# Kernel optimization log

Measured on AMD Instinct MI355X. Metric: run time of the kernel, lower is better.

The kernel has to match this reference:

```python
import jax, jax.numpy as jnp
import numpy as np

B, N, CACHE = 2, 2048, 512
D_MODEL, N_HEADS, HEAD_DIM, FF, KSZ = 768, 12, 64, 3072, 31
EPS = 1e-5


def rmsnorm(x, w):
    return x * jax.lax.rsqrt(jnp.mean(x * x, axis=-1, keepdims=True) + EPS) * w


def rope(x, pos):
    # x: [B, T, H, D], pos: [T] (absolute positions incl. cache offset)
    half = x.shape[-1] // 2
    inv = 1.0 / (10000.0 ** (jnp.arange(half, dtype=jnp.float32) / half))
    ang = pos.astype(jnp.float32)[:, None] * inv[None, :]           # [T, half]
    cos = jnp.concatenate([jnp.cos(ang), jnp.cos(ang)], -1)[None, :, None, :]
    sin = jnp.concatenate([jnp.sin(ang), jnp.sin(ang)], -1)[None, :, None, :]
    x1, x2 = x[..., :half], x[..., half:]
    rot = jnp.concatenate([-x2, x1], -1)
    return x * cos + rot * sin


def setup_inputs() -> dict:
    key = jax.random.key(0)
    ks = jax.random.split(key, 16)
    w = lambda k, shape: jax.random.normal(k, shape, jnp.float32) * 0.02
    kk = jax.random.split(ks[15], 16)
    return {
        "x": jax.random.normal(ks[0], (B, N, D_MODEL), jnp.float32),
        "attn_mask": jnp.ones((B, CACHE + N), bool),
        "pad_mask": jnp.zeros((B, N), bool),
        "length": N,
        "cached_kv": jax.random.normal(ks[1], (B, CACHE, 2, N_HEADS, HEAD_DIM), jnp.float32),
        "ff1_norm_w": jnp.ones((D_MODEL,), jnp.float32),
        "ff1_w1": w(ks[2], (D_MODEL, FF)), "ff1_b1": jnp.zeros((FF,), jnp.float32),
        "ff1_w2": w(ks[3], (FF, D_MODEL)), "ff1_b2": jnp.zeros((D_MODEL,), jnp.float32),
        "attn_norm_w": jnp.ones((D_MODEL,), jnp.float32),
        "qkv_w": w(ks[4], (D_MODEL, 3 * N_HEADS * HEAD_DIM)),
        "out_w": w(ks[5], (N_HEADS * HEAD_DIM, D_MODEL)),
        "q_norm_w": jnp.ones((HEAD_DIM,), jnp.float32),
        "k_norm_w": jnp.ones((HEAD_DIM,), jnp.float32),
        "conv_norm_w": jnp.ones((D_MODEL,), jnp.float32),
        "pw1_w": w(ks[6], (D_MODEL, 2 * D_MODEL)), "pw1_b": jnp.zeros((2 * D_MODEL,), jnp.float32),
        "dw_w": w(ks[7], (D_MODEL, KSZ)), "dw_b": jnp.zeros((D_MODEL,), jnp.float32),
        "bn_g": jnp.ones((D_MODEL,), jnp.float32), "bn_b": jnp.zeros((D_MODEL,), jnp.float32),
        "pw2_w": w(ks[8], (D_MODEL, D_MODEL)), "pw2_b": jnp.zeros((D_MODEL,), jnp.float32),
        "ff2_norm_w": jnp.ones((D_MODEL,), jnp.float32),
        "ff2_w1": w(kk[0], (D_MODEL, FF)), "ff2_b1": jnp.zeros((FF,), jnp.float32),
        "ff2_w2": w(kk[1], (FF, D_MODEL)), "ff2_b2": jnp.zeros((D_MODEL,), jnp.float32),
        "out_norm_w": jnp.ones((D_MODEL,), jnp.float32),
    }


def _ff(x, nw, w1, b1, w2, b2):
    h = jax.nn.gelu(rmsnorm(x, nw) @ w1 + b1)        # FusedMLP: gelu(tanh approx)
    return 0.5 * (h @ w2 + b2)                        # Scale(0.5, ...)


def _attention(x, pad_mask, attn_mask, cached_kv, nw, qkv_w, out_w, qnw, knw):
    y = rmsnorm(x, nw)
    y = jnp.where(pad_mask[..., None], 0.0, y)
    qkv = (y @ qkv_w).reshape(B, N, N_HEADS, HEAD_DIM, 3)  # (h d qkv) layout
    q, k, v = qkv[..., 0], qkv[..., 1], qkv[..., 2]
    q = rmsnorm(q, qnw)
    k = rmsnorm(k, knw)
    k_full = jnp.concatenate([cached_kv[:, :, 0], k], axis=1)  # [B, KV, H, D]
    v_full = jnp.concatenate([cached_kv[:, :, 1], v], axis=1)
    kv_to_cache = jnp.stack([k_full, v_full], axis=2)          # [B, KV, 2, H, D]
    kv_len = k_full.shape[1]
    pos = jnp.arange(kv_len)
    k_rot = rope(k_full, pos)
    q_rot = rope(q, pos[kv_len - N:])
    scale = 1.0 / jnp.sqrt(jnp.asarray(HEAD_DIM, jnp.float32))
    scores = jnp.einsum('bqhd,bkhd->bhqk', q_rot, k_rot) * scale
    scores = jnp.where(attn_mask[:, None, None, :], scores, jnp.finfo(scores.dtype).min)
    attn = jax.nn.softmax(scores, axis=-1)
    out = jnp.einsum('bhqk,bkhd->bqhd', attn, v_full).reshape(B, N, N_HEADS * HEAD_DIM)
    out = jnp.where(pad_mask[..., None], 0.0, out)
    return out @ out_w, kv_to_cache


def _conv(x, pad_mask, nw, pw1_w, pw1_b, dw_w, dw_b, bn_g, bn_b, pw2_w, pw2_b):
    y = rmsnorm(x, nw)
    y = jnp.where(pad_mask[..., None], 0.0, y)
    y = y @ pw1_w + pw1_b                             # pointwise conv1
    a, b = jnp.split(y, 2, axis=-1)
    y = a * jax.nn.sigmoid(b)                          # GLU
    rhs = dw_w.T[:, None, :]                           # [K, 1, C] (WIO, depthwise)
    y = jax.lax.conv_general_dilated(
        y, rhs, (1,), [(KSZ // 2, KSZ // 2)],
        dimension_numbers=('NWC', 'WIO', 'NWC'),
        feature_group_count=D_MODEL) + dw_b
    m = jnp.mean(y, axis=(0, 1))                       # batch(re)norm, train-mode stats
    v = jnp.var(y, axis=(0, 1))
    y = (y - m) * jax.lax.rsqrt(v + EPS) * bn_g + bn_b
    y = y * jax.nn.sigmoid(y)                          # SiLU
    return y @ pw2_w + pw2_b


def reference(x, attn_mask, pad_mask, length, cached_kv,
              ff1_norm_w, ff1_w1, ff1_b1, ff1_w2, ff1_b2,
              attn_norm_w, qkv_w, out_w, q_norm_w, k_norm_w,
              conv_norm_w, pw1_w, pw1_b, dw_w, dw_b, bn_g, bn_b, pw2_w, pw2_b,
              ff2_norm_w, ff2_w1, ff2_b1, ff2_w2, ff2_b2, out_norm_w):
    x = _ff(x, ff1_norm_w, ff1_w1, ff1_b1, ff1_w2, ff1_b2) + x
    attn_out, kv_to_cache = _attention(x, pad_mask, attn_mask, cached_kv,
                                       attn_norm_w, qkv_w, out_w, q_norm_w, k_norm_w)
    x = attn_out + x
    # NOTE: source code has no residual add around the conv block
    x = _conv(x, pad_mask, conv_norm_w, pw1_w, pw1_b, dw_w, dw_b, bn_g, bn_b, pw2_w, pw2_b)
    x = _ff(x, ff2_norm_w, ff2_w1, ff2_b1, ff2_w2, ff2_b2) + x
    x = rmsnorm(x, out_norm_w)
    return x, kv_to_cache
```

## Files before the change

### kernel.cpp

```cpp
#include <hip/hip_runtime.h>
#include <hip/hip_bf16.h>
#include <math.h>

namespace {
constexpr int Bc   = 2;
constexpr int Nn   = 2048;
constexpr int CACHE= 512;
constexpr int KVL  = 2560;
constexpr int DM   = 768;
constexpr int NH   = 12;
constexpr int HD   = 64;
constexpr int FFD  = 3072;
constexpr int RR   = Bc * Nn;
}
#define EPSF 1e-5f

typedef unsigned short u16;
typedef __bf16 bf16x8 __attribute__((ext_vector_type(8)));
typedef float  f32x4  __attribute__((ext_vector_type(4)));
typedef u16    u16x8  __attribute__((ext_vector_type(8)));
typedef u16    u16x4  __attribute__((ext_vector_type(4)));

#define GPTR(p) ((const __attribute__((address_space(1))) void*)(p))
#define LPTR(p) ((__attribute__((address_space(3))) void*)(p))

__device__ __forceinline__ float fast_exp2(float a) {
  float e;
  asm("v_exp_f32 %0, %1" : "=v"(e) : "v"(a));
  return e;
}
__device__ __forceinline__ float fast_rcp(float x) {
  float r;
  asm("v_rcp_f32 %0, %1" : "=v"(r) : "v"(x));
  return r;
}
__device__ __forceinline__ float geluf(float x) {
  const float u = 0.7978845608028654f * x * (1.0f + 0.044715f * x * x);
  const float e = fast_exp2(u * 2.885390081777927f);
  const float t = (e - 1.0f) * fast_rcp(e + 1.0f);
  return 0.5f * x * (1.0f + t);
}
__device__ __forceinline__ float sigmoidf_(float x) {
  const float e = fast_exp2(-x * 1.4426950408889634f);
  return fast_rcp(1.0f + e);
}
__device__ __forceinline__ u16 f2bf(float x) {
  union { float f; unsigned u; } v; v.f = x;
  unsigned r = (v.u + 0x7fffu + ((v.u >> 16) & 1u)) >> 16;
  return (u16)r;
}
__device__ __forceinline__ float bf2f(u16 u) {
  union { unsigned u; float f; } v; v.u = ((unsigned)u) << 16;
  return v.f;
}
__device__ __forceinline__ void rope_sc(float pos, int j, float* s, float* c) {
  const float e = fast_exp2(-(float)j * 0.41524101186092028f);
  const float rev = pos * (e * 0.15915494309189535f);
  const float fr = rev - floorf(rev);
  asm("v_sin_f32 %0, %1" : "=v"(*s) : "v"(fr));
  asm("v_cos_f32 %0, %1" : "=v"(*c) : "v"(fr));
}

template<bool BF>
__global__ __launch_bounds__(256) void k_rmsnorm2(const float* __restrict__ in,
                                                  const float* __restrict__ w,
                                                  void* __restrict__ outv) {
  const int row = blockIdx.x;
  const int t = threadIdx.x;
  const float4* x4 = (const float4*)(in + (size_t)row * DM);
  float4 v = make_float4(0.f, 0.f, 0.f, 0.f);
  float ss = 0.f;
  if (t < 192) {
    v = x4[t];
    ss = fmaf(v.x, v.x, fmaf(v.y, v.y, fmaf(v.z, v.z, v.w * v.w)));
  }
  __shared__ float red[5];
#pragma unroll
  for (int off = 32; off > 0; off >>= 1) ss += __shfl_down(ss, off, 64);
  if ((t & 63) == 0) red[t >> 6] = ss;
  __syncthreads();
  if (t == 0) red[4] = red[0] + red[1] + red[2] + red[3];
  __syncthreads();
  const float scale = rsqrtf(red[4] * (1.0f / (float)DM) + EPSF);
  if (t < 192) {
    const float4 wv = ((const float4*)w)[t];
    const float r0 = v.x * scale * wv.x;
    const float r1 = v.y * scale * wv.y;
    const float r2 = v.z * scale * wv.z;
    const float r3 = v.w * scale * wv.w;
    if (BF) {
      u16x4 o; o[0] = f2bf(r0); o[1] = f2bf(r1); o[2] = f2bf(r2); o[3] = f2bf(r3);
      ((u16x4*)outv)[(size_t)row * 192 + t] = o;
    } else {
      ((float4*)outv)[(size_t)row * 192 + t] = make_float4(r0, r1, r2, r3);
    }
  }
}

__device__ __forceinline__ void wt_tile(const float* __restrict__ W,
                                        u16* __restrict__ Wt, int K, int N,
                                        int gx, int r,
                                        u16 (*T)[72], int tid) {
  const int nb = (r % gx) * 64;
  const int kb = (r / gx) * 64;
#pragma unroll
  for (int p = 0; p < 4; ++p) {
    const int rr = p * 16 + (tid >> 4);
    const int c = (tid & 15) * 4;
    float4 v = *(const float4*)(W + (size_t)(kb + rr) * N + nb + c);
    T[c + 0][rr] = f2bf(v.x); T[c + 1][rr] = f2bf(v.y);
    T[c + 2][rr] = f2bf(v.z); T[c + 3][rr] = f2bf(v.w);
  }
  __syncthreads();
  const int cc = (tid & 7) * 8;
#pragma unroll
  for (int p = 0; p < 2; ++p) {
    const int rr = p * 32 + (tid >> 3);
    *(u16x8*)(Wt + (size_t)(nb + rr) * K + kb + cc) = *(const u16x8*)&T[rr][cc];
  }
}

__global__ __launch_bounds__(256) void k_wt_all(
    const float* w0, u16* o0,
    const float* w1, u16* o1,
    const float* w2, u16* o2,
    const float* w3, u16* o3,
    const float* w4, u16* o4,
    const float* w5, u16* o5,
    const float* w6, u16* o6,
    const float* w7, u16* o7,
    float* stats) {
  __shared__ __align__(16) u16 T[64][72];
  const int tid = threadIdx.x;
  int r = blockIdx.x;
  if (r < 576) { wt_tile(w0, o0, 768, 3072, 48, r, T, tid); return; } r -= 576;
  if (r < 576) { wt_tile(w1, o1, 3072, 768, 12, r, T, tid); return; } r -= 576;
  if (r < 432) { wt_tile(w2, o2, 768, 2304, 36, r, T, tid); return; } r -= 432;
  if (r < 144) { wt_tile(w3, o3, 768, 768, 12, r, T, tid); return; } r -= 144;
  if (r < 288) { wt_tile(w4, o4, 768, 1536, 24, r, T, tid); return; } r -= 288;
  if (r < 144) { wt_tile(w5, o5, 768, 768, 12, r, T, tid); return; } r -= 144;
  if (r < 576) { wt_tile(w6, o6, 768, 3072, 48, r, T, tid); return; } r -= 576;
  if (r < 576) { wt_tile(w7, o7, 3072, 768, 12, r, T, tid); return; } r -= 576;
  const int idx = r * 256 + tid;
  if (idx < 2 * DM) stats[idx] = 0.f;
}

template<int BM, int BN, int BKt, int MODE, bool OUTBF>
__global__ __launch_bounds__(256) void k_gemm_mfma(const u16* __restrict__ A,
                                                   const u16* __restrict__ Wt,
                                                   const float* __restrict__ bias,
                                                   const float* __restrict__ res,
                                                   void* __restrict__ Cv,
                                                   int K, int Nc) {
  constexpr int CH  = BKt / 8;
  constexpr int SWM = CH - 1;
  constexpr int RT  = BM / 32;
  constexpr int CT  = BN / 32;
  constexpr int KK  = BKt / 32;
  constexpr int ACH = BM * BKt / 8 / 256;
  constexpr int BCH = BN * BKt / 8 / 256;
  constexpr int LD  = ACH + BCH;
  static_assert(LD == 3 || LD == 4, "vmcnt ledger");
  __shared__ __align__(16) u16 As[3][BM * BKt];
  __shared__ __align__(16) u16 Bs[3][BN * BKt];
  const int tid  = threadIdx.x;
  const int lane = tid & 63;
  const int wbase = tid & 192;
  const int w    = tid >> 6;
  const int gx = gridDim.x;
  const int nwg = gx * gridDim.y;
  int bid = blockIdx.y * gx + blockIdx.x;
  if ((nwg & 7) == 0) bid = (bid & 7) * (nwg >> 3) + (bid >> 3);
  const int rowBase = (bid / gx) * BM;
  const int colBase = (bid % gx) * BN;
  const int l15 = lane & 15, quad = lane >> 4;
  const int wr = w >> 1, wc = w & 1;
  const int xsw = l15 & SWM;

  const u16* aS[ACH];
#pragma unroll
  for (int s = 0; s < ACH; ++s) {
    const int c = s * 256 + tid;
    const int r = c / CH;
    const int kc = (c & SWM) ^ (r & SWM);
    aS[s] = A + (size_t)(rowBase + r) * K + kc * 8;
  }
  const u16* bS[BCH];
#pragma unroll
  for (int s = 0; s < BCH; ++s) {
    const int c = s * 256 + tid;
    const int r = c / CH;
    const int kc = (c & SWM) ^ (r & SWM);
    bS[s] = Wt + (size_t)(colBase + r) * K + kc * 8;
  }

  f32x4 acc[RT][CT];
#pragma unroll
  for (int i = 0; i < RT; ++i)
#pragma unroll
    for (int j = 0; j < CT; ++j) acc[i][j] = (f32x4){0.f, 0.f, 0.f, 0.f};

  auto stage = [&](int buf, int k0e) {
#pragma unroll
    for (int s = 0; s < ACH; ++s)
      __builtin_amdgcn_global_load_lds(GPTR(aS[s] + k0e),
          LPTR((char*)As[buf] + (size_t)(s * 256 + wbase) * 16), 16, 0, 0);
#pragma unroll
    for (int s = 0; s < BCH; ++s)
      __builtin_amdgcn_global_load_lds(GPTR(bS[s] + k0e),
          LPTR((char*)Bs[buf] + (size_t)(s * 256 + wbase) * 16), 16, 0, 0);
  };

#define GEMM_STEP(BUF, I, DOSTAGE, LAST)                                           \
  {                                                                                \
    if (LAST) { asm volatile("s_waitcnt vmcnt(0)" ::: "memory"); }                 \
    else if (LD == 3) { asm volatile("s_waitcnt vmcnt(3)" ::: "memory"); }         \
    else { asm volatile("s_waitcnt vmcnt(4)" ::: "memory"); }                      \
    __builtin_amdgcn_s_barrier();                                                  \
    asm volatile("" ::: "memory");                                                 \
    if (DOSTAGE) stage(((BUF) + 2) % 3, ((I) + 2) * BKt);                          \
    const u16* ab = As[BUF];                                                       \
    const u16* bb = Bs[BUF];                                                       \
    _Pragma("unroll")                                                              \
    for (int kk = 0; kk < KK; ++kk) {                                              \
      bf16x8 aF[RT], bF[CT];                                                       \
      _Pragma("unroll")                                                            \
      for (int rt = 0; rt < RT; ++rt) {                                            \
        const int m = wr * (BM / 2) + rt * 16 + l15;                               \
        aF[rt] = *(const bf16x8*)&ab[m * BKt + (((kk * 4 + quad) ^ xsw) * 8)];     \
      }                                                                            \
      _Pragma("unroll")                                                            \
      for (int ct = 0; ct < CT; ++ct) {                                            \
        const int n = wc * (BN / 2) + ct * 16 + l15;                               \
        bF[ct] = *(const bf16x8*)&bb[n * BKt + (((kk * 4 + quad) ^ xsw) * 8)];     \
      }                                                                            \
      _Pragma("unroll")                                                            \
      for (int rt = 0; rt < RT; ++rt)                                              \
        _Pragma("unroll")                                                          \
        for (int ct = 0; ct < CT; ++ct)                                            \
          acc[rt][ct] = __builtin_amdgcn_mfma_f32_16x16x32_bf16(bF[ct], aF[rt],    \
                                                                acc[rt][ct],       \
                                                                0, 0, 0);          \
    }                                                                              \
  }

  const int nsteps = K / BKt;
  stage(0, 0);
  stage(1, BKt);
  int i = 0;
  for (; i < nsteps - 3; i += 3) {
    GEMM_STEP(0, i + 0, true, false);
    GEMM_STEP(1, i + 1, true, false);
    GEMM_STEP(2, i + 2, true, false);
  }
  GEMM_STEP(0, nsteps - 3, true, false);
  GEMM_STEP(1, nsteps - 2, false, false);
  GEMM_STEP(2, nsteps - 1, false, true);
#undef GEMM_STEP

#pragma unroll
  for (int ct = 0; ct < CT; ++ct) {
    const int n0 = colBase + wc * (BN / 2) + ct * 16 + quad * 4;
    float b0 = 0.f, b1 = 0.f, b2 = 0.f, b3 = 0.f;
    if (bias) {
      const float4 bv = *(const float4*)(bias + n0);
      b0 = bv.x; b1 = bv.y; b2 = bv.z; b3 = bv.w;
    }
#pragma unroll
    for (int rt = 0; rt < RT; ++rt) {
      const int m = rowBase + wr * (BM / 2) + rt * 16 + l15;
      float v0 = acc[rt][ct][0] + b0;
      float v1 = acc[rt][ct][1] + b1;
      float v2 = acc[rt][ct][2] + b2;
      float v3 = acc[rt][ct][3] + b3;
      if (MODE == 1) {
        v0 = geluf(v0); v1 = geluf(v1); v2 = geluf(v2); v3 = geluf(v3);
      } else if (MODE == 2) {
        const float4 rv = *(const float4*)(res + (size_t)m * Nc + n0);
        v0 = 0.5f * v0 + rv.x; v1 = 0.5f * v1 + rv.y;
        v2 = 0.5f * v2 + rv.z; v3 = 0.5f * v3 + rv.w;
      } else if (MODE == 3) {
        const float4 rv = *(const float4*)(res + (size_t)m * Nc + n0);
        v0 += rv.x; v1 += rv.y; v2 += rv.z; v3 += rv.w;
      }
      if (OUTBF) {
        unsigned w0, w1;
        asm("v_cvt_pk_bf16_f32 %0, %1, %2" : "=v"(w0) : "v"(v0), "v"(v1));
        asm("v_cvt_pk_bf16_f32 %0, %1, %2" : "=v"(w1) : "v"(v2), "v"(v3));
        uint2 st; st.x = w0; st.y = w1;
        *(uint2*)((u16*)Cv + (size_t)m * Nc + n0) = st;
      } else {
        *(float4*)((float*)Cv + (size_t)m * Nc + n0) =
            make_float4(v0, v1, v2, v3);
      }
    }
  }
}

__global__ __launch_bounds__(768) void k_qkv_post(const float* __restrict__ qkv,
                                                  const float* __restrict__ qw,
                                                  const float* __restrict__ kw,
                                                  u16* __restrict__ qbf,
                                                  u16* __restrict__ krotbf,
                                                  float* __restrict__ kvout) {
  const int row = blockIdx.x;
  const int b = row >> 11;
  const int n = row & 2047;
  const int h = threadIdx.x >> 6;
  const int d = threadIdx.x & 63;
  const float* src = qkv + (size_t)row * (3 * DM) + h * 192 + d * 3;
  const float q = src[0], k = src[1], v = src[2];
  float sq = q * q, sk = k * k;
#pragma unroll
  for (int off = 32; off > 0; off >>= 1) {
    sq += __shfl_xor(sq, off, 64);
    sk += __shfl_xor(sk, off, 64);
  }
  const float qs = rsqrtf(sq * (1.0f / 64.0f) + EPSF);
  const float ks = rsqrtf(sk * (1.0f / 64.0f) + EPSF);
  const float qn = q * qs * qw[d];
  const float kn = k * ks * kw[d];
  const size_t kvbase = ((size_t)b * KVL + (CACHE + n)) * (2 * DM) + h * 64 + d;
  kvout[kvbase] = kn;
  kvout[kvbase + DM] = v;
  const int j = d & 31;
  float s, c;
  rope_sc((float)(CACHE + n), j, &s, &c);
  const float oq = __shfl_xor(qn, 32, 64);
  const float ok = __shfl_xor(kn, 32, 64);
  const float rq = (d < 32) ? -oq : oq;
  const float rk = (d < 32) ? -ok : ok;
  qbf[((size_t)row * NH + h) * 64 + d] = f2bf((qn * c + rq * s) * 0.18033688011112042f);
  krotbf[((size_t)(b * KVL + CACHE + n) * NH + h) * 64 + d] = f2bf(kn * c + rk * s);
}

__global__ __launch_bounds__(768) void k_cache_prep(const float* __restrict__ cached,
                                                    float* __restrict__ kvout,
                                                    u16* __restrict__ krotbf) {
  const int row = blockIdx.x;
  const int b = row / CACHE, t = row - b * CACHE;
  const int h = threadIdx.x >> 6;
  const int d = threadIdx.x & 63;
  const float k = cached[((size_t)row * 2 + 0) * DM + h * 64 + d];
  const float v = cached[((size_t)row * 2 + 1) * DM + h * 64 + d];
  const size_t kb = ((size_t)b * KVL + t) * (2 * DM) + h * 64 + d;
  kvout[kb] = k;
  kvout[kb + DM] = v;
  const int j = d & 31;
  float s, c;
  rope_sc((float)t, j, &s, &c);
  const float ok = __shfl_xor(k, 32, 64);
  const float rk = (d < 32) ? -ok : ok;
  krotbf[((size_t)(b * KVL + t) * NH + h) * 64 + d] = f2bf(k * c + rk * s);
}

__global__ __launch_bounds__(256) void k_vt(const float* __restrict__ kvout,
                                            u16* __restrict__ vtbf) {
  __shared__ __align__(16) u16 T[64][72];
  const int bh = blockIdx.x / 40;
  const int tb = blockIdx.x % 40;
  const int b = bh / NH, h = bh % NH;
  const int t0 = tb * 64;
  {
    const int tloc = threadIdx.x >> 2;
    const int dg = (threadIdx.x & 3) * 16;
    const float* src = kvout + ((size_t)b * KVL + t0 + tloc) * (2 * DM) + DM + h * 64 + dg;
    float4 v0 = *(const float4*)(src);
    float4 v1 = *(const float4*)(src + 4);
    float4 v2 = *(const float4*)(src + 8);
    float4 v3 = *(const float4*)(src + 12);
    T[dg + 0][tloc] = f2bf(v0.x);  T[dg + 1][tloc] = f2bf(v0.y);
    T[dg + 2][tloc] = f2bf(v0.z);  T[dg + 3][tloc] = f2bf(v0.w);
    T[dg + 4][tloc] = f2bf(v1.x);  T[dg + 5][tloc] = f2bf(v1.y);
    T[dg + 6][tloc] = f2bf(v1.z);  T[dg + 7][tloc] = f2bf(v1.w);
    T[dg + 8][tloc] = f2bf(v2.x);  T[dg + 9][tloc] = f2bf(v2.y);
    T[dg + 10][tloc] = f2bf(v2.z); T[dg + 11][tloc] = f2bf(v2.w);
    T[dg + 12][tloc] = f2bf(v3.x); T[dg + 13][tloc] = f2bf(v3.y);
    T[dg + 14][tloc] = f2bf(v3.z); T[dg + 15][tloc] = f2bf(v3.w);
  }
  __syncthreads();
  const int d = threadIdx.x >> 2;
  const int kg = (threadIdx.x & 3) * 16;
  u16x8 a = *(const u16x8*)&T[d][kg];
  u16x8 b8 = *(const u16x8*)&T[d][kg + 8];
  u16* dst = vtbf + ((size_t)(b * NH + h) * 64 + d) * KVL + t0 + kg;
  *(u16x8*)dst = a;
  *(u16x8*)(dst + 8) = b8;
}

__global__ __launch_bounds__(256) void k_attn3(const u16* __restrict__ qbf,
                                               const u16* __restrict__ krotbf,
                                               const u16* __restrict__ vtbf,
                                               u16* __restrict__ attnout) {
  __shared__ __align__(16) char smem[49152];
  u16* const KsB = (u16*)smem;
  u16* const VsB = (u16*)(smem + 24576);
  const int lane = threadIdx.x & 63;
  const int wid  = threadIdx.x >> 6;
  const int bid = blockIdx.x;
  const int swz = (bid & 7) * (768 / 8) + (bid >> 3);
  const int qblk = swz & 31;
  const int bh   = swz >> 5;
  const int b = bh / NH, h = bh % NH;
  const int q0 = qblk * 64 + wid * 16;
  const int l15 = lane & 15;
  const int quad = lane >> 4;
  const int sw = l15 & 7;

  const u16* qp = qbf + ((size_t)(b * Nn + q0 + l15) * NH + h) * 64 + quad * 8;
  const bf16x8 bQ0 = *(const bf16x8*)qp;
  const bf16x8 bQ1 = *(const bf16x8*)(qp + 32);
  asm volatile("" :: "v"(*(const f32x4*)&bQ0), "v"(*(const f32x4*)&bQ1));

  f32x4 O[4] = {};
  float l_lane = 0.f;

  const int c0 = (wid * 2 + 0) * 64 + lane;
  const int c1 = (wid * 2 + 1) * 64 + lane;
  const int r0 = c0 >> 3, kc0 = (c0 & 7) ^ (r0 & 7);
  const int r1 = c1 >> 3, kc1 = (c1 & 7) ^ (r1 & 7);
  const int g0 = (r0 & 3) | ((r0 & 0xC) << 1) | ((r0 & 0x10) >> 2) | (r0 & 0x20);
  const int g1 = (r1 & 3) | ((r1 & 0xC) << 1) | ((r1 & 0x10) >> 2) | (r1 & 0x20);
  const u16* kbase = krotbf + ((size_t)b * KVL * NH + h) * 64;
  const u16* vbase = vtbf + ((size_t)(b * NH + h) * 64) * KVL;
  const u16* ksrc0 = kbase + (size_t)g0 * (NH * 64) + kc0 * 8;
  const u16* ksrc1 = kbase + (size_t)g1 * (NH * 64) + kc1 * 8;
  const u16* vsrc0 = vbase + (size_t)r0 * KVL + kc0 * 8;
  const u16* vsrc1 = vbase + (size_t)r1 * KVL + kc1 * 8;
  const size_t kd0 = (size_t)(wid * 2 + 0) * 1024;
  const size_t kd1 = (size_t)(wid * 2 + 1) * 1024;

  auto stage = [&](int buf, int tile) {
    char* kd = (char*)KsB + buf * 8192;
    char* vd = (char*)VsB + buf * 8192;
    const size_t koff = (size_t)tile * (64 * NH * 64);
    const int voff = tile * 64;
    __builtin_amdgcn_global_load_lds(GPTR(ksrc0 + koff), LPTR(kd + kd0), 16, 0, 0);
    __builtin_amdgcn_global_load_lds(GPTR(vsrc0 + voff), LPTR(vd + kd0), 16, 0, 0);
    __builtin_amdgcn_global_load_lds(GPTR(ksrc1 + koff), LPTR(kd + kd1), 16, 0, 0);
    __builtin_amdgcn_global_load_lds(GPTR(vsrc1 + voff), LPTR(vd + kd1), 16, 0, 0);
  };

#define ATTN_TILE(BI, I, DOSTAGE, LAST)                                            \
  {                                                                                \
    if (LAST) { asm volatile("s_waitcnt vmcnt(0)" ::: "memory"); }                 \
    else      { asm volatile("s_waitcnt vmcnt(4)" ::: "memory"); }                 \
    __builtin_amdgcn_s_barrier();                                                  \
    asm volatile("" ::: "memory");                                                 \
    if (DOSTAGE) stage(((BI) + 2) % 3, (I) + 2);                                   \
    const u16* ksc = KsB + (BI) * 4096;                                            \
    const u16* vsc = VsB + (BI) * 4096;                                            \
    unsigned Pr[2][4];                                                             \
    _Pragma("unroll")                                                              \
    for (int nt = 0; nt < 4; ++nt) {                                               \
      const int krow = nt * 16 + l15;                                              \
      const bf16x8 aK0 = *(const bf16x8*)&ksc[krow * 64 + ((quad ^ sw) * 8)];      \
      const bf16x8 aK1 = *(const bf16x8*)&ksc[krow * 64 + (((4 + quad) ^ sw) * 8)];\
      f32x4 cc = {};                                                               \
      cc = __builtin_amdgcn_mfma_f32_16x16x32_bf16(aK0, bQ0, cc, 0, 0, 0);         \
      cc = __builtin_amdgcn_mfma_f32_16x16x32_bf16(aK1, bQ1, cc, 0, 0, 0);         \
      const float p0 = fast_exp2(cc[0]);                                           \
      const float p1 = fast_exp2(cc[1]);                                           \
      const float p2 = fast_exp2(cc[2]);                                           \
      const float p3 = fast_exp2(cc[3]);                                           \
      l_lane += (p0 + p1) + (p2 + p3);                                             \
      asm("v_cvt_pk_bf16_f32 %0, %1, %2"                                           \
          : "=v"(Pr[nt >> 1][(nt & 1) * 2 + 0]) : "v"(p0), "v"(p1));               \
      asm("v_cvt_pk_bf16_f32 %0, %1, %2"                                           \
          : "=v"(Pr[nt >> 1][(nt & 1) * 2 + 1]) : "v"(p2), "v"(p3));               \
    }                                                                              \
    __builtin_amdgcn_s_setprio(1);                                                 \
    _Pragma("unroll")                                                              \
    for (int kt = 0; kt < 2; ++kt) {                                               \
      union { unsigned u[4]; bf16x8 v; } pu;                                       \
      pu.u[0] = Pr[kt][0]; pu.u[1] = Pr[kt][1];                                    \
      pu.u[2] = Pr[kt][2]; pu.u[3] = Pr[kt][3];                                    \
      _Pragma("unroll")                                                            \
      for (int ot = 0; ot < 4; ++ot) {                                             \
        const int vrow = ot * 16 + l15;                                            \
        const bf16x8 aV =                                                          \
            *(const bf16x8*)&vsc[vrow * 64 + (((kt * 4 + quad) ^ sw) * 8)];        \
        O[ot] = __builtin_amdgcn_mfma_f32_16x16x32_bf16(aV, pu.v, O[ot], 0, 0, 0); \
      }                                                                            \
    }                                                                              \
    __builtin_amdgcn_s_setprio(0);                                                 \
  }

  stage(0, 0);
  stage(1, 1);
  for (int j = 0; j < 12; ++j) {
    const int i0 = j * 3;
    ATTN_TILE(0, i0 + 0, true, false);
    ATTN_TILE(1, i0 + 1, true, false);
    ATTN_TILE(2, i0 + 2, true, false);
  }
  ATTN_TILE(0, 36, true, false);
  ATTN_TILE(1, 37, true, false);
  ATTN_TILE(2, 38, false, false);
  ATTN_TILE(0, 39, false, true);
#undef ATTN_TILE

  l_lane += __shfl_xor(l_lane, 16, 64);
  l_lane += __shfl_xor(l_lane, 32, 64);
  const float il = 1.0f / l_lane;
  __builtin_amdgcn_s_barrier();
  asm volatile("" ::: "memory");
  float* const OF  = (float*)smem;
  float* const ILs = (float*)(smem + 17408);
  if (quad == 0) ILs[wid * 16 + l15] = il;
  float* of = OF + (size_t)(wid * 16 + l15) * 68;
#pragma unroll
  for (int ot = 0; ot < 4; ++ot)
    *(f32x4*)&of[ot * 16 + quad * 4] = O[ot];
  asm volatile("s_waitcnt lgkmcnt(0)" ::: "memory");
  const int q  = lane >> 2;
  const int dg = (lane & 3) * 16;
  const float sc = ILs[wid * 16 + q];
  const float* srcp = OF + (size_t)(wid * 16 + q) * 68 + dg;
  unsigned wv[8];
#pragma unroll
  for (int i2 = 0; i2 < 8; ++i2) {
    const float a0 = srcp[2 * i2] * sc;
    const float a1 = srcp[2 * i2 + 1] * sc;
    asm("v_cvt_pk_bf16_f32 %0, %1, %2" : "=v"(wv[i2]) : "v"(a0), "v"(a1));
  }
  u16* dst = attnout + ((size_t)(b * Nn + q0 + q)) * DM + h * 64 + dg;
  uint4 s0; s0.x = wv[0]; s0.y = wv[1]; s0.z = wv[2]; s0.w = wv[3];
  uint4 s1; s1.x = wv[4]; s1.y = wv[5]; s1.z = wv[6]; s1.w = wv[7];
  *(uint4*)dst = s0;
  *(uint4*)(dst + 8) = s1;
}

__global__ __launch_bounds__(256) void k_dwconv2(const u16* __restrict__ pw1,
                                                 const float* __restrict__ w,
                                                 const float* __restrict__ bsd,
                                                 float* __restrict__ out,
                                                 float* __restrict__ stats) {
  __shared__ float S[94][68];
  __shared__ float Wl[31][64];
  const int cb = blockIdx.x * 64;
  const int n0 = blockIdx.y * 64;
  const int b  = blockIdx.z;
  for (int idx = threadIdx.x; idx < 94 * 16; idx += 256) {
    const int r = idx >> 4, cg = (idx & 15) * 4;
    const int n = n0 - 15 + r;
    float4 v = make_float4(0.f, 0.f, 0.f, 0.f);
    if (n >= 0 && n < Nn) {
      const u16* p = pw1 + ((size_t)(b * Nn + n)) * (2 * DM) + cb + cg;
      u16x4 av = *(const u16x4*)(p);
      u16x4 gv = *(const u16x4*)(p + DM);
      v.x = bf2f(av[0]) * sigmoidf_(bf2f(gv[0]));
      v.y = bf2f(av[1]) * sigmoidf_(bf2f(gv[1]));
      v.z = bf2f(av[2]) * sigmoidf_(bf2f(gv[2]));
      v.w = bf2f(av[3]) * sigmoidf_(bf2f(gv[3]));
    }
    *(float4*)&S[r][cg] = v;
  }
  for (int idx = threadIdx.x; idx < 31 * 64; idx += 256) {
    const int c = idx & 63, tap = idx >> 6;
    Wl[tap][c] = w[(size_t)(cb + c) * 31 + tap];
  }
  __syncthreads();

  const int cg  = (threadIdx.x & 15) * 4;
  const int nl0 = threadIdx.x >> 4;
  const float4 b4 = *(const float4*)(bsd + cb + cg);
  float sum[4] = {0.f, 0.f, 0.f, 0.f};
  float sq[4]  = {0.f, 0.f, 0.f, 0.f};
#pragma unroll
  for (int p = 0; p < 4; ++p) {
    const int nl = p * 16 + nl0;
    float a0 = b4.x, a1 = b4.y, a2 = b4.z, a3 = b4.w;
#pragma unroll
    for (int t = 0; t < 31; ++t) {
      const float4 sv = *(const float4*)&S[nl + t][cg];
      const float4 wv = *(const float4*)&Wl[t][cg & 63];
      a0 = fmaf(sv.x, wv.x, a0); a1 = fmaf(sv.y, wv.y, a1);
      a2 = fmaf(sv.z, wv.z, a2); a3 = fmaf(sv.w, wv.w, a3);
    }
    *(float4*)(out + ((size_t)(b * Nn + n0 + nl)) * DM + cb + cg) =
        make_float4(a0, a1, a2, a3);
    sum[0] += a0; sum[1] += a1; sum[2] += a2; sum[3] += a3;
    sq[0] = fmaf(a0, a0, sq[0]); sq[1] = fmaf(a1, a1, sq[1]);
    sq[2] = fmaf(a2, a2, sq[2]); sq[3] = fmaf(a3, a3, sq[3]);
  }
  __syncthreads();
  *(float4*)&S[nl0][cg]      = make_float4(sum[0], sum[1], sum[2], sum[3]);
  *(float4*)&S[16 + nl0][cg] = make_float4(sq[0], sq[1], sq[2], sq[3]);
  __syncthreads();
  if (threadIdx.x < 64) {
    const int c = threadIdx.x;
    float s = 0.f, q = 0.f;
#pragma unroll
    for (int i = 0; i < 16; ++i) { s += S[i][c]; q += S[16 + i][c]; }
    atomicAdd(&stats[cb + c], s);
    atomicAdd(&stats[DM + cb + c], q);
  }
}

__global__ __launch_bounds__(256) void k_bn_apply(const float* __restrict__ x,
                                                  const float* __restrict__ stats,
                                                  const float* __restrict__ g,
                                                  const float* __restrict__ bb,
                                                  u16* __restrict__ out) {
  const int idx = blockIdx.x * 256 + threadIdx.x;
  const int c = idx % DM;
  const float mean = stats[c] * (1.0f / (float)RR);
  const float var = stats[DM + c] * (1.0f / (float)RR) - mean * mean;
  float y = (x[idx] - mean) * rsqrtf(var + EPSF) * g[c] + bb[c];
  out[idx] = f2bf(y * sigmoidf_(y));
}

extern "C" void kernel_launch(void* const* d_in, const int* in_sizes, int n_in,
                              void* d_out, int out_size, void* d_ws, size_t ws_size,
                              hipStream_t stream) {
  const float* x       = (const float*)d_in[0];
  const float* cached  = (const float*)d_in[4];
  const float* ff1_nw  = (const float*)d_in[5];
  const float* ff1_w1  = (const float*)d_in[6];
  const float* ff1_b1  = (const float*)d_in[7];
  const float* ff1_w2  = (const float*)d_in[8];
  const float* ff1_b2  = (const float*)d_in[9];
  const float* attn_nw = (const float*)d_in[10];
  const float* qkv_w   = (const float*)d_in[11];
  const float* out_w   = (const float*)d_in[12];
  const float* q_nw    = (const float*)d_in[13];
  const float* k_nw    = (const float*)d_in[14];
  const float* conv_nw = (const float*)d_in[15];
  const float* pw1_w   = (const float*)d_in[16];
  const float* pw1_b   = (const float*)d_in[17];
  const float* dw_w    = (const float*)d_in[18];
  const float* dw_b    = (const float*)d_in[19];
  const float* bn_g    = (const float*)d_in[20];
  const float* bn_b    = (const float*)d_in[21];
  const float* pw2_w   = (const float*)d_in[22];
  const float* pw2_b   = (const float*)d_in[23];
  const float* ff2_nw  = (const float*)d_in[24];
  const float* ff2_w1  = (const float*)d_in[25];
  const float* ff2_b1  = (const float*)d_in[26];
  const float* ff2_w2  = (const float*)d_in[27];
  const float* ff2_b2  = (const float*)d_in[28];
  const float* out_nw  = (const float*)d_in[29];

  float* out_x  = (float*)d_out;
  float* out_kv = out_x + (size_t)RR * DM;

  u16* wt_ff1w1 = (u16*)d_ws;
  u16* wt_ff1w2 = wt_ff1w1 + (size_t)3072 * 768;
  u16* wt_qkv   = wt_ff1w2 + (size_t)768 * 3072;
  u16* wt_out   = wt_qkv   + (size_t)2304 * 768;
  u16* wt_pw1   = wt_out   + (size_t)768 * 768;
  u16* wt_pw2   = wt_pw1   + (size_t)1536 * 768;
  u16* wt_ff2w1 = wt_pw2   + (size_t)768 * 768;
  u16* wt_ff2w2 = wt_ff2w1 + (size_t)3072 * 768;
  u16* abuf     = wt_ff2w2 + (size_t)768 * 3072;
  u16* hbuf     = abuf + (size_t)RR * DM;
  float* xA     = (float*)(hbuf + (size_t)RR * FFD);
  float* xB     = xA + (size_t)RR * DM;
  float* qkvbuf = xB + (size_t)RR * DM;
  u16* qbf      = (u16*)(qkvbuf + (size_t)RR * 3 * DM);
  u16* krotbf   = qbf + (size_t)RR * DM;
  u16* vtbf     = krotbf + (size_t)Bc * KVL * DM;
  float* bn_stats = (float*)(vtbf + (size_t)Bc * KVL * DM);
  u16* attnout  = (u16*)qkvbuf;
  float* dwout  = qkvbuf;
  u16* bnout    = (u16*)(qkvbuf + (size_t)RR * DM);

  const dim3 blk(256);
  k_wt_all<<<3318, blk, 0, stream>>>(ff1_w1, wt_ff1w1, ff1_w2, wt_ff1w2,
                                     qkv_w, wt_qkv, out_w, wt_out,
                                     pw1_w, wt_pw1, pw2_w, wt_pw2,
                                     ff2_w1, wt_ff2w1, ff2_w2, wt_ff2w2,
                                     bn_stats);

  k_rmsnorm2<true><<<RR, blk, 0, stream>>>(x, ff1_nw, abuf);
  k_gemm_mfma<128, 128, 32, 1, true><<<dim3(FFD / 128, RR / 128), blk, 0, stream>>>(
      abuf, wt_ff1w1, ff1_b1, nullptr, hbuf, DM, FFD);
  k_gemm_mfma<64, 64, 64, 2, false><<<dim3(DM / 64, RR / 64), blk, 0, stream>>>(
      hbuf, wt_ff1w2, ff1_b2, x, xA, FFD, DM);
  k_rmsnorm2<true><<<RR, blk, 0, stream>>>(xA, attn_nw, abuf);
  k_gemm_mfma<128, 128, 32, 0, false><<<dim3(3 * DM / 128, RR / 128), blk, 0, stream>>>(
      abuf, wt_qkv, nullptr, nullptr, qkvbuf, DM, 3 * DM);
  k_qkv_post<<<RR, 768, 0, stream>>>(qkvbuf, q_nw, k_nw, qbf, krotbf, out_kv);
  k_cache_prep<<<Bc * CACHE, 768, 0, stream>>>(cached, out_kv, krotbf);
  k_vt<<<Bc * NH * (KVL / 64), blk, 0, stream>>>(out_kv, vtbf);
  k_attn3<<<Bc * NH * (Nn / 64), blk, 0, stream>>>(qbf, krotbf, vtbf, attnout);
  k_gemm_mfma<64, 64, 64, 3, false><<<dim3(DM / 64, RR / 64), blk, 0, stream>>>(
      attnout, wt_out, nullptr, xA, xB, DM, DM);
  k_rmsnorm2<true><<<RR, blk, 0, stream>>>(xB, conv_nw, abuf);
  k_gemm_mfma<64, 128, 32, 0, true><<<dim3(2 * DM / 128, RR / 64), blk, 0, stream>>>(
      abuf, wt_pw1, pw1_b, nullptr, hbuf, DM, 2 * DM);
  k_dwconv2<<<dim3(DM / 64, Nn / 64, Bc), blk, 0, stream>>>(hbuf, dw_w, dw_b,
                                                            dwout, bn_stats);
  k_bn_apply<<<RR * DM / 256, blk, 0, stream>>>(dwout, bn_stats, bn_g, bn_b, bnout);
  k_gemm_mfma<64, 64, 64, 0, false><<<dim3(DM / 64, RR / 64), blk, 0, stream>>>(
      bnout, wt_pw2, pw2_b, nullptr, xA, DM, DM);
  k_rmsnorm2<true><<<RR, blk, 0, stream>>>(xA, ff2_nw, abuf);
  k_gemm_mfma<128, 128, 32, 1, true><<<dim3(FFD / 128, RR / 128), blk, 0, stream>>>(
      abuf, wt_ff2w1, ff2_b1, nullptr, hbuf, DM, FFD);
  k_gemm_mfma<64, 64, 64, 2, false><<<dim3(DM / 64, RR / 64), blk, 0, stream>>>(
      hbuf, wt_ff2w2, ff2_b2, xA, xB, FFD, DM);
  k_rmsnorm2<false><<<RR, blk, 0, stream>>>(xB, out_nw, out_x);
}
```

Baseline: 493.3 us.

## Fuse attention prep kernels, compute softmax row sums via MFMA, raise GEMM MFMA priority

Merges the qkv post-processing, cache preparation and V-transpose kernels into one launch, with the transpose reading V straight from the qkv and cache inputs instead of from the kv output. This removes two launches and the dependency on the kv write. In attention, the softmax denominator is now accumulated with an MFMA against a vector of ones, replacing per-lane scalar adds and the final cross-lane shuffles. GEMM inner loops also raise wave priority around the MFMA block. The fused prep kernel's transpose reads strided scalar loads from qkv, which may be less coalesced than before.

```diff
diff --git a/kernel.cpp b/kernel.cpp
--- a/kernel.cpp
+++ b/kernel.cpp
@@ -234,6 +234,7 @@
         const int n = wc * (BN / 2) + ct * 16 + l15;                               \
         bF[ct] = *(const bf16x8*)&bb[n * BKt + (((kk * 4 + quad) ^ xsw) * 8)];     \
       }                                                                            \
+      __builtin_amdgcn_s_setprio(1);                                               \
       _Pragma("unroll")                                                            \
       for (int rt = 0; rt < RT; ++rt)                                              \
         _Pragma("unroll")                                                          \
@@ -241,6 +242,7 @@
           acc[rt][ct] = __builtin_amdgcn_mfma_f32_16x16x32_bf16(bF[ct], aF[rt],    \
                                                                 acc[rt][ct],       \
                                                                 0, 0, 0);          \
+      __builtin_amdgcn_s_setprio(0);                                               \
     }                                                                              \
   }
 
@@ -297,95 +299,85 @@
   }
 }
 
-__global__ __launch_bounds__(768) void k_qkv_post(const float* __restrict__ qkv,
-                                                  const float* __restrict__ qw,
-                                                  const float* __restrict__ kw,
-                                                  u16* __restrict__ qbf,
-                                                  u16* __restrict__ krotbf,
-                                                  float* __restrict__ kvout) {
-  const int row = blockIdx.x;
-  const int b = row >> 11;
-  const int n = row & 2047;
-  const int h = threadIdx.x >> 6;
-  const int d = threadIdx.x & 63;
-  const float* src = qkv + (size_t)row * (3 * DM) + h * 192 + d * 3;
-  const float q = src[0], k = src[1], v = src[2];
-  float sq = q * q, sk = k * k;
-#pragma unroll
-  for (int off = 32; off > 0; off >>= 1) {
-    sq += __shfl_xor(sq, off, 64);
-    sk += __shfl_xor(sk, off, 64);
-  }
-  const float qs = rsqrtf(sq * (1.0f / 64.0f) + EPSF);
-  const float ks = rsqrtf(sk * (1.0f / 64.0f) + EPSF);
-  const float qn = q * qs * qw[d];
-  const float kn = k * ks * kw[d];
-  const size_t kvbase = ((size_t)b * KVL + (CACHE + n)) * (2 * DM) + h * 64 + d;
-  kvout[kvbase] = kn;
-  kvout[kvbase + DM] = v;
-  const int j = d & 31;
-  float s, c;
-  rope_sc((float)(CACHE + n), j, &s, &c);
-  const float oq = __shfl_xor(qn, 32, 64);
-  const float ok = __shfl_xor(kn, 32, 64);
-  const float rq = (d < 32) ? -oq : oq;
-  const float rk = (d < 32) ? -ok : ok;
-  qbf[((size_t)row * NH + h) * 64 + d] = f2bf((qn * c + rq * s) * 0.18033688011112042f);
-  krotbf[((size_t)(b * KVL + CACHE + n) * NH + h) * 64 + d] = f2bf(kn * c + rk * s);
-}
-
-__global__ __launch_bounds__(768) void k_cache_prep(const float* __restrict__ cached,
-                                                    float* __restrict__ kvout,
-                                                    u16* __restrict__ krotbf) {
-  const int row = blockIdx.x;
-  const int b = row / CACHE, t = row - b * CACHE;
-  const int h = threadIdx.x >> 6;
-  const int d = threadIdx.x & 63;
-  const float k = cached[((size_t)row * 2 + 0) * DM + h * 64 + d];
-  const float v = cached[((size_t)row * 2 + 1) * DM + h * 64 + d];
-  const size_t kb = ((size_t)b * KVL + t) * (2 * DM) + h * 64 + d;
-  kvout[kb] = k;
-  kvout[kb + DM] = v;
-  const int j = d & 31;
-  float s, c;
-  rope_sc((float)t, j, &s, &c);
-  const float ok = __shfl_xor(k, 32, 64);
-  const float rk = (d < 32) ? -ok : ok;
-  krotbf[((size_t)(b * KVL + t) * NH + h) * 64 + d] = f2bf(k * c + rk * s);
-}
-
-__global__ __launch_bounds__(256) void k_vt(const float* __restrict__ kvout,
-                                            u16* __restrict__ vtbf) {
+__global__ __launch_bounds__(768) void k_attn_prep(const float* __restrict__ qkv,
+                                                   const float* __restrict__ cached,
+                                                   const float* __restrict__ qw,
+                                                   const float* __restrict__ kw,
+                                                   u16* __restrict__ qbf,
+                                                   u16* __restrict__ krotbf,
+                                                   float* __restrict__ kvout,
+                                                   u16* __restrict__ vtbf) {
   __shared__ __align__(16) u16 T[64][72];
-  const int bh = blockIdx.x / 40;
-  const int tb = blockIdx.x % 40;
+  const int tid = threadIdx.x;
+  int r = blockIdx.x;
+  if (r < RR) {
+    const int b = r >> 11;
+    const int n = r & 2047;
+    const int h = tid >> 6;
+    const int d = tid & 63;
+    const float* src = qkv + (size_t)r * (3 * DM) + h * 192 + d * 3;
+    const float q = src[0], k = src[1], v = src[2];
+    float sq = q * q, sk = k * k;
+#pragma unroll
+    for (int off = 32; off > 0; off >>= 1) {
+      sq += __shfl_xor(sq, off, 64);
+      sk += __shfl_xor(sk, off, 64);
+    }
+    const float qs = rsqrtf(sq * (1.0f / 64.0f) + EPSF);
+    const float ks = rsqrtf(sk * (1.0f / 64.0f) + EPSF);
+    const float qn = q * qs * qw[d];
+    const float kn = k * ks * kw[d];
+    const size_t kvbase = ((size_t)b * KVL + (CACHE + n)) * (2 * DM) + h * 64 + d;
+    kvout[kvbase] = kn;
+    kvout[kvbase + DM] = v;
+    const int j = d & 31;
+    float s, c;
+    rope_sc((float)(CACHE + n), j, &s, &c);
+    const float oq = __shfl_xor(qn, 32, 64);
+    const float ok = __shfl_xor(kn, 32, 64);
+    const float rq = (d < 32) ? -oq : oq;
+    const float rk = (d < 32) ? -ok : ok;
+    qbf[((size_t)r * NH + h) * 64 + d] = f2bf((qn * c + rq * s) * 0.18033688011112042f);
+    krotbf[((size_t)(b * KVL + CACHE + n) * NH + h) * 64 + d] = f2bf(kn * c + rk * s);
+    return;
+  }
+  r -= RR;
+  if (r < Bc * CACHE) {
+    const int b = r / CACHE, t = r - b * CACHE;
+    const int h = tid >> 6;
+    const int d = tid & 63;
+    const float k = cached[((size_t)r * 2 + 0) * DM + h * 64 + d];
+    const float v = cached[((size_t)r * 2 + 1) * DM + h * 64 + d];
+    const size_t kb = ((size_t)b * KVL + t) * (2 * DM) + h * 64 + d;
+    kvout[kb] = k;
+    kvout[kb + DM] = v;
+    const int j = d & 31;
+    float s, c;
+    rope_sc((float)t, j, &s, &c);
+    const float ok = __shfl_xor(k, 32, 64);
+    const float rk = (d < 32) ? -ok : ok;
+    krotbf[((size_t)(b * KVL + t) * NH + h) * 64 + d] = f2bf(k * c + rk * s);
+    return;
+  }
+  r -= Bc * CACHE;
+  const int bh = r / (KVL / 64);
+  const int tb = r % (KVL / 64);
   const int b = bh / NH, h = bh % NH;
   const int t0 = tb * 64;
-  {
-    const int tloc = threadIdx.x >> 2;
-    const int dg = (threadIdx.x & 3) * 16;
-    const float* src = kvout + ((size_t)b * KVL + t0 + tloc) * (2 * DM) + DM + h * 64 + dg;
-    float4 v0 = *(const float4*)(src);
-    float4 v1 = *(const float4*)(src + 4);
-    float4 v2 = *(const float4*)(src + 8);
-    float4 v3 = *(const float4*)(src + 12);
-    T[dg + 0][tloc] = f2bf(v0.x);  T[dg + 1][tloc] = f2bf(v0.y);
-    T[dg + 2][tloc] = f2bf(v0.z);  T[dg + 3][tloc] = f2bf(v0.w);
-    T[dg + 4][tloc] = f2bf(v1.x);  T[dg + 5][tloc] = f2bf(v1.y);
-    T[dg + 6][tloc] = f2bf(v1.z);  T[dg + 7][tloc] = f2bf(v1.w);
-    T[dg + 8][tloc] = f2bf(v2.x);  T[dg + 9][tloc] = f2bf(v2.y);
-    T[dg + 10][tloc] = f2bf(v2.z); T[dg + 11][tloc] = f2bf(v2.w);
-    T[dg + 12][tloc] = f2bf(v3.x); T[dg + 13][tloc] = f2bf(v3.y);
-    T[dg + 14][tloc] = f2bf(v3.z); T[dg + 15][tloc] = f2bf(v3.w);
+  for (int idx = tid; idx < 4096; idx += 768) {
+    const int tt = idx >> 6, d = idx & 63;
+    const int tg = t0 + tt;
+    float v;
+    if (tg < CACHE) v = cached[((size_t)(b * CACHE + tg) * 2 + 1) * DM + h * 64 + d];
+    else v = qkv[(size_t)(b * Nn + tg - CACHE) * (3 * DM) + h * 192 + d * 3 + 2];
+    T[d][tt] = f2bf(v);
   }
   __syncthreads();
-  const int d = threadIdx.x >> 2;
-  const int kg = (threadIdx.x & 3) * 16;
-  u16x8 a = *(const u16x8*)&T[d][kg];
-  u16x8 b8 = *(const u16x8*)&T[d][kg + 8];
-  u16* dst = vtbf + ((size_t)(b * NH + h) * 64 + d) * KVL + t0 + kg;
-  *(u16x8*)dst = a;
-  *(u16x8*)(dst + 8) = b8;
+  if (tid < 512) {
+    const int d = tid >> 3, kg = (tid & 7) * 8;
+    *(u16x8*)(vtbf + ((size_t)(b * NH + h) * 64 + d) * KVL + t0 + kg) =
+        *(const u16x8*)&T[d][kg];
+  }
 }
 
 __global__ __launch_bounds__(256) void k_attn3(const u16* __restrict__ qbf,
@@ -411,6 +403,11 @@
   const bf16x8 bQ0 = *(const bf16x8*)qp;
   const bf16x8 bQ1 = *(const bf16x8*)(qp + 32);
   asm volatile("" :: "v"(*(const f32x4*)&bQ0), "v"(*(const f32x4*)&bQ1));
+
+  union { u16x8 u; bf16x8 v; } ones_u;
+#pragma unroll
+  for (int z = 0; z < 8; ++z) ones_u.u[z] = 0x3F80;
+  const bf16x8 aOnes = ones_u.v;
 
   f32x4 O[4] = {};
   float l_lane = 0.f;
@@ -463,18 +460,19 @@
       const float p1 = fast_exp2(cc[1]);                                           \
       const float p2 = fast_exp2(cc[2]);                                           \
       const float p3 = fast_exp2(cc[3]);                                           \
-      l_lane += (p0 + p1) + (p2 + p3);                                             \
       asm("v_cvt_pk_bf16_f32 %0, %1, %2"                                           \
           : "=v"(Pr[nt >> 1][(nt & 1) * 2 + 0]) : "v"(p0), "v"(p1));               \
       asm("v_cvt_pk_bf16_f32 %0, %1, %2"                                           \
           : "=v"(Pr[nt >> 1][(nt & 1) * 2 + 1]) : "v"(p2), "v"(p3));               \
     }                                                                              \
     __builtin_amdgcn_s_setprio(1);                                                 \
+    f32x4 ccl = {};                                                                \
     _Pragma("unroll")                                                              \
     for (int kt = 0; kt < 2; ++kt) {                                               \
       union { unsigned u[4]; bf16x8 v; } pu;                                       \
       pu.u[0] = Pr[kt][0]; pu.u[1] = Pr[kt][1];                                    \
       pu.u[2] = Pr[kt][2]; pu.u[3] = Pr[kt][3];                                    \
+      ccl = __builtin_amdgcn_mfma_f32_16x16x32_bf16(aOnes, pu.v, ccl, 0, 0, 0);    \
       _Pragma("unroll")                                                            \
       for (int ot = 0; ot < 4; ++ot) {                                             \
         const int vrow = ot * 16 + l15;                                            \
@@ -484,6 +482,7 @@
       }                                                                            \
     }                                                                              \
     __builtin_amdgcn_s_setprio(0);                                                 \
+    l_lane += ccl[0];                                                              \
   }
 
   stage(0, 0);
@@ -500,8 +499,6 @@
   ATTN_TILE(0, 39, false, true);
 #undef ATTN_TILE
 
-  l_lane += __shfl_xor(l_lane, 16, 64);
-  l_lane += __shfl_xor(l_lane, 32, 64);
   const float il = 1.0f / l_lane;
   __builtin_amdgcn_s_barrier();
   asm volatile("" ::: "memory");
@@ -681,9 +678,8 @@
   k_rmsnorm2<true><<<RR, blk, 0, stream>>>(xA, attn_nw, abuf);
   k_gemm_mfma<128, 128, 32, 0, false><<<dim3(3 * DM / 128, RR / 128), blk, 0, stream>>>(
       abuf, wt_qkv, nullptr, nullptr, qkvbuf, DM, 3 * DM);
-  k_qkv_post<<<RR, 768, 0, stream>>>(qkvbuf, q_nw, k_nw, qbf, krotbf, out_kv);
-  k_cache_prep<<<Bc * CACHE, 768, 0, stream>>>(cached, out_kv, krotbf);
-  k_vt<<<Bc * NH * (KVL / 64), blk, 0, stream>>>(out_kv, vtbf);
+  k_attn_prep<<<RR + Bc * CACHE + Bc * NH * (KVL / 64), 768, 0, stream>>>(
+      qkvbuf, cached, q_nw, k_nw, qbf, krotbf, out_kv, vtbf);
   k_attn3<<<Bc * NH * (Nn / 64), blk, 0, stream>>>(qbf, krotbf, vtbf, attnout);
   k_gemm_mfma<64, 64, 64, 3, false><<<dim3(DM / 64, RR / 64), blk, 0, stream>>>(
       attnout, wt_out, nullptr, xA, xB, DM, DM);
```

Measured after the change: 512.8 us. +4.0%, slower.
